# Kernel optimization log

Measured on AMD Instinct MI355X. Metric: run time of the kernel, lower is better.

The kernel has to match this reference:

```python
import jax, jax.numpy as jnp
import numpy as np

SEQ, BATCH, IN_DIM, HID, LAYERS, OUT = 512, 64, 512, 1024, 4, 1


def setup_inputs() -> dict:
    key = jax.random.key(0)
    ks = jax.random.split(key, 8)
    s = 1.0 / np.sqrt(HID)  # PyTorch default init range
    u = lambda k, shape: jax.random.uniform(k, shape, jnp.float32, -s, s)
    return {
        "x": jax.random.normal(ks[0], (SEQ, BATCH, IN_DIM), jnp.float32),
        "w_ih0": u(ks[1], (4 * HID, IN_DIM)),
        "w_ih_rest": u(ks[2], (LAYERS - 1, 4 * HID, HID)),
        "w_hh": u(ks[3], (LAYERS, 4 * HID, HID)),
        "b_ih": u(ks[4], (LAYERS, 4 * HID)),
        "b_hh": u(ks[5], (LAYERS, 4 * HID)),
        "fc_w": u(ks[6], (OUT, HID)),
        "fc_b": u(ks[7], (OUT,)),
    }


def _lstm_layer(xs, w_ih, w_hh, b):
    # xs: [T, B, D]; PyTorch gate order: i, f, g, o
    T, B, _ = xs.shape
    H = w_hh.shape[1]
    gx = jnp.einsum("tbd,gd->tbg", xs, w_ih) + b  # precompute input GEMM [T,B,4H]

    def step(carry, g_t):
        h, c = carry
        g = g_t + h @ w_hh.T
        i, f, gg, o = jnp.split(g, 4, axis=-1)
        c = jax.nn.sigmoid(f) * c + jax.nn.sigmoid(i) * jnp.tanh(gg)
        h = jax.nn.sigmoid(o) * jnp.tanh(c)
        return (h, c), h

    init = (jnp.zeros((B, H), xs.dtype), jnp.zeros((B, H), xs.dtype))
    _, hs = jax.lax.scan(step, init, gx)
    return hs  # [T, B, H]


def reference(x, w_ih0, w_ih_rest, w_hh, b_ih, b_hh, fc_w, fc_b):
    h = _lstm_layer(x, w_ih0, w_hh[0], b_ih[0] + b_hh[0])
    for l in range(1, LAYERS):
        h = _lstm_layer(h, w_ih_rest[l - 1], w_hh[l], b_ih[l] + b_hh[l])
    # Faithful to original: output is seq-first [T,B,H], and x[:, -1, :]
    # selects the LAST BATCH element over all timesteps -> [T, H]
    last = jax.nn.sigmoid(h[:, -1, :])
    return last @ fc_w.T + fc_b  # [T, OUT]
```

## Files before the change

### kernel.cpp

```cpp
#include <hip/hip_runtime.h>


typedef unsigned short u16;
typedef short bf16x8 __attribute__((ext_vector_type(8)));
typedef float f32x4 __attribute__((ext_vector_type(4)));
typedef float f32x16 __attribute__((ext_vector_type(16)));

__device__ __forceinline__ u16 f2bf(float f) {
  unsigned u = __float_as_uint(f);
  return (u16)((u + 0x7FFFu + ((u >> 16) & 1u)) >> 16);
}
__device__ __forceinline__ float bf2f(u16 s) {
  return __uint_as_float(((unsigned)s) << 16);
}
__device__ __forceinline__ bf16x8 ld8(const u16* p) {
  uint4 v = *(const uint4*)p;
  return __builtin_bit_cast(bf16x8, v);
}
__device__ __forceinline__ float sigf(float x) {
  x = fminf(fmaxf(x, -30.f), 30.f);
  return 1.f / (1.f + __expf(-x));
}
__device__ __forceinline__ float tanhf_(float x) {
  x = fminf(fmaxf(x, -15.f), 15.f);
  float e = __expf(-2.f * x);
  return (1.f - e) / (1.f + e);
}

#define AT_LD(p) __hip_atomic_load((p), __ATOMIC_RELAXED, __HIP_MEMORY_SCOPE_AGENT)
#define AT_ST(p, v) __hip_atomic_store((p), (v), __ATOMIC_RELAXED, __HIP_MEMORY_SCOPE_AGENT)

__global__ void repack_w(const float* __restrict__ wih0, const float* __restrict__ wihr,
                         const float* __restrict__ whh, u16* __restrict__ WCAT) {
  size_t i = (size_t)blockIdx.x * 256 + threadIdx.x;
  int l = (int)(i >> 23);
  int r = (int)(i >> 11) & 4095;
  int c = (int)i & 2047;
  int Kx = l ? 1024 : 512;
  float v = 0.f;
  if (c < Kx) v = l ? wihr[((size_t)(l - 1) * 4096 + r) * 1024 + c]
                    : wih0[(size_t)r * 512 + c];
  else if (c < Kx + 1024) v = whh[((size_t)l * 4096 + r) * 1024 + (c - Kx)];
  WCAT[i] = f2bf(v);
}

__global__ void repack_x(const float* __restrict__ x, u16* __restrict__ XP) {
  int i = blockIdx.x * 256 + threadIdx.x;
  int t = i >> 12, r = i & 4095, kc = r >> 6, b = r & 63;
  const float* src = x + ((size_t)t * 64 + b) * 512 + kc * 8;
  float4 v0 = *(const float4*)src, v1 = *(const float4*)(src + 4);
  u16 o[8] = {f2bf(v0.x), f2bf(v0.y), f2bf(v0.z), f2bf(v0.w),
              f2bf(v1.x), f2bf(v1.y), f2bf(v1.z), f2bf(v1.w)};
  *(uint4*)(XP + ((size_t)(t * 64 + kc) * 64 + b) * 8) = *(uint4*)o;
}

__global__ void bias_add(const float* __restrict__ a, const float* __restrict__ b,
                         float* __restrict__ o) {
  int i = blockIdx.x * blockDim.x + threadIdx.x;
  o[i] = a[i] + b[i];
}

template <int NF, int FX>
__device__ __forceinline__ void run_pipe(
    int layer, int w64, const u16* __restrict__ WCAT, const u16* __restrict__ XP,
    u16* __restrict__ HR, u16* __restrict__ HOUT, const float* __restrict__ BIAS,
    unsigned* __restrict__ FLAG, unsigned* __restrict__ EPOCH, float* R) {
  const int tid = threadIdx.x;
  const int lane = tid & 63, wv = tid >> 6;
  const int ks = wv & 3, nh = wv >> 2;
  const int l31 = lane & 31, lhi = lane >> 5;
  const int W = layer * 64 + w64;

  bf16x8 wf[NF];
  {
    const int lr = nh * 32 + l31;
    const int grow = (lr >> 4) * 1024 + 16 * w64 + (lr & 15);
    const u16* wrow = WCAT + ((size_t)layer * 4096 + grow) * 2048;
#pragma unroll
    for (int kk = 0; kk < NF; ++kk) {
      int f = ks * NF + kk;
      wf[kk] = ld8(wrow + f * 16 + lhi * 8);
    }
  }

  const int u = tid & 15, bp = tid >> 4;
  const int col = 16 * w64 + u;
  float c0 = 0.f, c1 = 0.f;
  const float bi = BIAS[layer * 4096 + col];
  const float bf_ = BIAS[layer * 4096 + 1024 + col];
  const float bg = BIAS[layer * 4096 + 2048 + col];
  const float bo = BIAS[layer * 4096 + 3072 + col];

  const int lane_base = (lhi * 64 + l31) * 8;
  u16* HRL = HR + (size_t)layer * 2097152;
  const u16* M0B = (NF == 32) ? HR + (size_t)(layer - 1) * 2097152 : XP;
  const int lrD = nh * 32 + l31;

  for (int s = 0; s < 515; ++s) {
    const int t = s - layer;
    const bool active = (t >= 0) && (t < 512);
    if (active) {
      *(f32x4*)&R[tid * 8] = f32x4{0.f, 0.f, 0.f, 0.f};
      *(f32x4*)&R[tid * 8 + 4] = f32x4{0.f, 0.f, 0.f, 0.f};
      __syncthreads();

      const u16* P0 = M0B + ((NF == 32) ? (size_t)(t & 31) * 65536
                                        : (size_t)t * 32768) + lane_base;
      const u16* P1 = HRL + (size_t)((t - 1) & 31) * 65536 + lane_base - (size_t)FX * 1024;

      f32x16 acc0 = {}, acc1 = {};
      uint4 a0[4], a1[4];
#pragma unroll
      for (int p = 0; p < 4; ++p) {
        int f = ks * NF + p;
        const u16* ap = (f < FX ? P0 : P1) + (size_t)f * 1024;
        a0[p] = *(const uint4*)ap;
        a1[p] = *(const uint4*)(ap + 256);
      }
#pragma unroll
      for (int kk = 0; kk < NF; ++kk) {
        uint4 ca = a0[kk & 3], cb = a1[kk & 3];
        if (kk + 4 < NF) {
          int f = ks * NF + kk + 4;
          const u16* ap = (f < FX ? P0 : P1) + (size_t)f * 1024;
          a0[kk & 3] = *(const uint4*)ap;
          a1[kk & 3] = *(const uint4*)(ap + 256);
        }
        acc0 = __builtin_amdgcn_mfma_f32_32x32x16_bf16(
            __builtin_bit_cast(bf16x8, ca), wf[kk], acc0, 0, 0, 0);
        acc1 = __builtin_amdgcn_mfma_f32_32x32x16_bf16(
            __builtin_bit_cast(bf16x8, cb), wf[kk], acc1, 0, 0, 0);
      }
#pragma unroll
      for (int r = 0; r < 16; ++r) {
        int m = (r & 3) + 8 * (r >> 2) + 4 * lhi;
        atomicAdd(&R[m * 64 + lrD], acc0[r]);
        atomicAdd(&R[(32 + m) * 64 + lrD], acc1[r]);
      }
      __syncthreads();
      {
        float p0i = R[bp * 64 + u] + bi, p0f = R[bp * 64 + 16 + u] + bf_;
        float p0g = R[bp * 64 + 32 + u] + bg, p0o = R[bp * 64 + 48 + u] + bo;
        float p1i = R[(bp + 32) * 64 + u] + bi, p1f = R[(bp + 32) * 64 + 16 + u] + bf_;
        float p1g = R[(bp + 32) * 64 + 32 + u] + bg, p1o = R[(bp + 32) * 64 + 48 + u] + bo;
        c0 = sigf(p0f) * c0 + sigf(p0i) * tanhf_(p0g);
        float h0 = sigf(p0o) * tanhf_(c0);
        c1 = sigf(p1f) * c1 + sigf(p1i) * tanhf_(p1g);
        float h1 = sigf(p1o) * tanhf_(c1);
        u16 hb0 = f2bf(h0), hb1 = f2bf(h1);
        unsigned n0 = (unsigned)(u16)__shfl_down((int)(unsigned)hb0, 1, 64);
        unsigned n1 = (unsigned)(u16)__shfl_down((int)(unsigned)hb1, 1, 64);
        if ((u & 1) == 0) {
          unsigned pk0 = (unsigned)hb0 | (n0 << 16);
          unsigned pk1 = (unsigned)hb1 | (n1 << 16);
          u16* slot = HRL + (size_t)(t & 31) * 65536;
          size_t e0 = ((size_t)(col >> 3) * 64 + bp) * 8 + (col & 7);
          AT_ST((unsigned*)(slot + e0), pk0);
          AT_ST((unsigned*)(slot + e0 + 256), pk1);
          if (layer == 3 && bp == 31)
            *(unsigned*)(HOUT + (size_t)t * 1024 + col) = pk1;
        }
      }
      __syncthreads();
    }
    const unsigned tgt = (unsigned)(s + 1);
    if (tid == 0) AT_ST(&FLAG[W * 64], tgt);
    if (W == 0) {
      if (wv == 0) {
        for (;;) {
          unsigned f0 = AT_LD(&FLAG[lane * 64]);
          unsigned f1 = AT_LD(&FLAG[(lane + 64) * 64]);
          unsigned f2 = AT_LD(&FLAG[(lane + 128) * 64]);
          unsigned f3 = AT_LD(&FLAG[(lane + 192) * 64]);
          bool ok = (f0 >= tgt) & (f1 >= tgt) & (f2 >= tgt) & (f3 >= tgt);
          if (__ballot(ok) == ~0ull) break;
          __builtin_amdgcn_s_sleep(1);
        }
        if (lane < 32) AT_ST(&EPOCH[lane * 64], tgt);
      }
    } else if (wv == 0) {
      unsigned* ep = &EPOCH[(W & 31) * 64];
      while (AT_LD(ep) < tgt) __builtin_amdgcn_s_sleep(1);
    }
    __syncthreads();
  }
}

__global__ __launch_bounds__(512, 2) void lstm_pipe(
    const u16* __restrict__ WCAT, const u16* __restrict__ XP,
    u16* __restrict__ HR, u16* __restrict__ HOUT,
    const float* __restrict__ BIAS, unsigned* __restrict__ FLAG,
    unsigned* __restrict__ EPOCH) {
  __shared__ float R[64 * 64];
  const int w = blockIdx.x;
  const int layer = w >> 6, w64 = w & 63;
  if (layer == 0) run_pipe<24, 32>(0, w64, WCAT, XP, HR, HOUT, BIAS, FLAG, EPOCH, R);
  else            run_pipe<32, 64>(layer, w64, WCAT, XP, HR, HOUT, BIAS, FLAG, EPOCH, R);
}

__global__ void lstm_head(const u16* __restrict__ Hl, const float* __restrict__ fcw,
                          const float* __restrict__ fcb, float* __restrict__ out) {
  int t = blockIdx.x, tid = threadIdx.x;
  const u16* hrow = Hl + (size_t)t * 1024;
  float s = 0.f;
  for (int j = tid; j < 1024; j += 256)
    s += sigf(bf2f(hrow[j])) * fcw[j];
  for (int o = 32; o; o >>= 1) s += __shfl_down(s, o, 64);
  __shared__ float red[4];
  if ((tid & 63) == 0) red[tid >> 6] = s;
  __syncthreads();
  if (tid == 0) out[t] = red[0] + red[1] + red[2] + red[3] + fcb[0];
}

extern "C" void kernel_launch(void* const* d_in, const int* in_sizes, int n_in,
                              void* d_out, int out_size, void* d_ws, size_t ws_size,
                              hipStream_t stream) {
  const float* x    = (const float*)d_in[0];
  const float* wih0 = (const float*)d_in[1];
  const float* wihr = (const float*)d_in[2];
  const float* whh  = (const float*)d_in[3];
  const float* bih  = (const float*)d_in[4];
  const float* bhh  = (const float*)d_in[5];
  const float* fcw  = (const float*)d_in[6];
  const float* fcb  = (const float*)d_in[7];
  float* out = (float*)d_out;

  char* ws = (char*)d_ws;
  size_t off = 0;
  auto alc = [&](size_t b) { void* p = ws + off; off = (off + b + 255) & ~(size_t)255; return p; };
  u16* WCAT  = (u16*)alc(33554432ull * 2);
  u16* XP    = (u16*)alc(16777216ull * 2);
  u16* HR    = (u16*)alc(8388608ull * 2);
  u16* HOUT  = (u16*)alc(524288ull * 2);
  float* BIAS = (float*)alc(16384 * 4);
  unsigned* FLAG  = (unsigned*)alc(256 * 64 * 4);
  unsigned* EPOCH = (unsigned*)alc(32 * 64 * 4);
  (void)ws_size; (void)in_sizes; (void)n_in; (void)out_size;

  hipMemsetAsync(HR, 0, 8388608ull * 2, stream);
  hipMemsetAsync(FLAG, 0, 256 * 64 * 4, stream);
  hipMemsetAsync(EPOCH, 0, 32 * 64 * 4, stream);
  repack_w<<<dim3(131072), 256, 0, stream>>>(wih0, wihr, whh, WCAT);
  repack_x<<<dim3(8192), 256, 0, stream>>>(x, XP);
  bias_add<<<dim3(64), 256, 0, stream>>>(bih, bhh, BIAS);

  void* args[] = {&WCAT, &XP, &HR, &HOUT, &BIAS, &FLAG, &EPOCH};
  hipLaunchCooperativeKernel((const void*)lstm_pipe, dim3(256), dim3(512),
                             args, 0, stream);

  lstm_head<<<dim3(512), 256, 0, stream>>>(HOUT, fcw, fcb, out);
}
```

Measured before the change: 14.78 ms.

## Replace global grid barrier with per-layer dataflow flags in LSTM wavefront pipeline

Removes the centralized per-step grid barrier, where block 0 polled all flags and broadcast an epoch. Each block now waits only on its own layer's flags from the previous step, the next layer's ring-buffer consumption (a 31-step slack window), and the previous layer's flag for the current step. It also splits the GEMM so the recurrent h@W_hh part runs before waiting on the lower layer's output, overlapping that wait with compute. Block-to-layer mapping is interleaved, and weight fragments are reordered into recurrent and input parts. The risks are spin-wait contention from busy polling without sleep, and correctness depending on the ring-buffer slack logic.

```diff
diff --git a/kernel.cpp b/kernel.cpp
--- a/kernel.cpp
+++ b/kernel.cpp
@@ -60,27 +60,26 @@
   o[i] = a[i] + b[i];
 }
 
-template <int NF, int FX>
+template <int NFX>
 __device__ __forceinline__ void run_pipe(
     int layer, int w64, const u16* __restrict__ WCAT, const u16* __restrict__ XP,
     u16* __restrict__ HR, u16* __restrict__ HOUT, const float* __restrict__ BIAS,
-    unsigned* __restrict__ FLAG, unsigned* __restrict__ EPOCH, float* R) {
+    unsigned* __restrict__ FLAG, float* R) {
   const int tid = threadIdx.x;
   const int lane = tid & 63, wv = tid >> 6;
   const int ks = wv & 3, nh = wv >> 2;
   const int l31 = lane & 31, lhi = lane >> 5;
-  const int W = layer * 64 + w64;
-
-  bf16x8 wf[NF];
+  const int FX = NFX * 4;
+
+  bf16x8 wfc[NFX], wfo[16];
   {
     const int lr = nh * 32 + l31;
     const int grow = (lr >> 4) * 1024 + 16 * w64 + (lr & 15);
     const u16* wrow = WCAT + ((size_t)layer * 4096 + grow) * 2048;
 #pragma unroll
-    for (int kk = 0; kk < NF; ++kk) {
-      int f = ks * NF + kk;
-      wf[kk] = ld8(wrow + f * 16 + lhi * 8);
-    }
+    for (int j = 0; j < NFX; ++j) wfc[j] = ld8(wrow + (j * 4 + ks) * 16 + lhi * 8);
+#pragma unroll
+    for (int j = 0; j < 16; ++j) wfo[j] = ld8(wrow + (FX + j * 4 + ks) * 16 + lhi * 8);
   }
 
   const int u = tid & 15, bp = tid >> 4;
@@ -93,109 +92,121 @@
 
   const int lane_base = (lhi * 64 + l31) * 8;
   u16* HRL = HR + (size_t)layer * 2097152;
-  const u16* M0B = (NF == 32) ? HR + (size_t)(layer - 1) * 2097152 : XP;
+  const u16* HRm1 = (layer > 0) ? HR + (size_t)(layer - 1) * 2097152 : XP;
   const int lrD = nh * 32 + l31;
 
-  for (int s = 0; s < 515; ++s) {
-    const int t = s - layer;
-    const bool active = (t >= 0) && (t < 512);
-    if (active) {
-      *(f32x4*)&R[tid * 8] = f32x4{0.f, 0.f, 0.f, 0.f};
-      *(f32x4*)&R[tid * 8 + 4] = f32x4{0.f, 0.f, 0.f, 0.f};
-      __syncthreads();
-
-      const u16* P0 = M0B + ((NF == 32) ? (size_t)(t & 31) * 65536
-                                        : (size_t)t * 32768) + lane_base;
-      const u16* P1 = HRL + (size_t)((t - 1) & 31) * 65536 + lane_base - (size_t)FX * 1024;
-
-      f32x16 acc0 = {}, acc1 = {};
+  for (int t = 0; t < 512; ++t) {
+    *(f32x4*)&R[tid * 8] = f32x4{0.f, 0.f, 0.f, 0.f};
+    *(f32x4*)&R[tid * 8 + 4] = f32x4{0.f, 0.f, 0.f, 0.f};
+    if (wv == 0) {
+      for (;;) {
+        int f1 = (int)AT_LD(&FLAG[layer * 64 + lane]);
+        bool ok = (f1 >= t);
+        if (layer < 3) {
+          int f2 = (int)AT_LD(&FLAG[(layer + 1) * 64 + lane]);
+          ok &= (f2 >= t - 31);
+        }
+        if (__ballot(ok) == ~0ull) break;
+      }
+    }
+    __syncthreads();
+
+    f32x16 acc0 = {}, acc1 = {};
+    {
+      const u16* PO = HRL + (size_t)((t - 1) & 31) * 65536 + lane_base;
       uint4 a0[4], a1[4];
 #pragma unroll
       for (int p = 0; p < 4; ++p) {
-        int f = ks * NF + p;
-        const u16* ap = (f < FX ? P0 : P1) + (size_t)f * 1024;
-        a0[p] = *(const uint4*)ap;
-        a1[p] = *(const uint4*)(ap + 256);
-      }
-#pragma unroll
-      for (int kk = 0; kk < NF; ++kk) {
-        uint4 ca = a0[kk & 3], cb = a1[kk & 3];
-        if (kk + 4 < NF) {
-          int f = ks * NF + kk + 4;
-          const u16* ap = (f < FX ? P0 : P1) + (size_t)f * 1024;
-          a0[kk & 3] = *(const uint4*)ap;
-          a1[kk & 3] = *(const uint4*)(ap + 256);
+        const u16* ap = PO + (size_t)(p * 4 + ks) * 1024;
+        a0[p] = *(const uint4*)ap; a1[p] = *(const uint4*)(ap + 256);
+      }
+#pragma unroll
+      for (int j = 0; j < 16; ++j) {
+        uint4 ca = a0[j & 3], cb = a1[j & 3];
+        if (j + 4 < 16) {
+          const u16* ap = PO + (size_t)((j + 4) * 4 + ks) * 1024;
+          a0[j & 3] = *(const uint4*)ap; a1[j & 3] = *(const uint4*)(ap + 256);
         }
         acc0 = __builtin_amdgcn_mfma_f32_32x32x16_bf16(
-            __builtin_bit_cast(bf16x8, ca), wf[kk], acc0, 0, 0, 0);
+            __builtin_bit_cast(bf16x8, ca), wfo[j], acc0, 0, 0, 0);
         acc1 = __builtin_amdgcn_mfma_f32_32x32x16_bf16(
-            __builtin_bit_cast(bf16x8, cb), wf[kk], acc1, 0, 0, 0);
-      }
-#pragma unroll
-      for (int r = 0; r < 16; ++r) {
-        int m = (r & 3) + 8 * (r >> 2) + 4 * lhi;
-        atomicAdd(&R[m * 64 + lrD], acc0[r]);
-        atomicAdd(&R[(32 + m) * 64 + lrD], acc1[r]);
-      }
-      __syncthreads();
-      {
-        float p0i = R[bp * 64 + u] + bi, p0f = R[bp * 64 + 16 + u] + bf_;
-        float p0g = R[bp * 64 + 32 + u] + bg, p0o = R[bp * 64 + 48 + u] + bo;
-        float p1i = R[(bp + 32) * 64 + u] + bi, p1f = R[(bp + 32) * 64 + 16 + u] + bf_;
-        float p1g = R[(bp + 32) * 64 + 32 + u] + bg, p1o = R[(bp + 32) * 64 + 48 + u] + bo;
-        c0 = sigf(p0f) * c0 + sigf(p0i) * tanhf_(p0g);
-        float h0 = sigf(p0o) * tanhf_(c0);
-        c1 = sigf(p1f) * c1 + sigf(p1i) * tanhf_(p1g);
-        float h1 = sigf(p1o) * tanhf_(c1);
-        u16 hb0 = f2bf(h0), hb1 = f2bf(h1);
-        unsigned n0 = (unsigned)(u16)__shfl_down((int)(unsigned)hb0, 1, 64);
-        unsigned n1 = (unsigned)(u16)__shfl_down((int)(unsigned)hb1, 1, 64);
-        if ((u & 1) == 0) {
-          unsigned pk0 = (unsigned)hb0 | (n0 << 16);
-          unsigned pk1 = (unsigned)hb1 | (n1 << 16);
-          u16* slot = HRL + (size_t)(t & 31) * 65536;
-          size_t e0 = ((size_t)(col >> 3) * 64 + bp) * 8 + (col & 7);
-          AT_ST((unsigned*)(slot + e0), pk0);
-          AT_ST((unsigned*)(slot + e0 + 256), pk1);
-          if (layer == 3 && bp == 31)
-            *(unsigned*)(HOUT + (size_t)t * 1024 + col) = pk1;
+            __builtin_bit_cast(bf16x8, cb), wfo[j], acc1, 0, 0, 0);
+      }
+    }
+    if (layer > 0 && wv == 0) {
+      for (;;) {
+        int f = (int)AT_LD(&FLAG[(layer - 1) * 64 + lane]);
+        if (__ballot(f >= t + 1) == ~0ull) break;
+      }
+    }
+    __syncthreads();
+    {
+      const u16* PC = HRm1 + ((layer > 0) ? (size_t)(t & 31) * 65536
+                                          : (size_t)t * 32768) + lane_base;
+      uint4 a0[4], a1[4];
+#pragma unroll
+      for (int p = 0; p < 4; ++p) {
+        const u16* ap = PC + (size_t)(p * 4 + ks) * 1024;
+        a0[p] = *(const uint4*)ap; a1[p] = *(const uint4*)(ap + 256);
+      }
+#pragma unroll
+      for (int j = 0; j < NFX; ++j) {
+        uint4 ca = a0[j & 3], cb = a1[j & 3];
+        if (j + 4 < NFX) {
+          const u16* ap = PC + (size_t)((j + 4) * 4 + ks) * 1024;
+          a0[j & 3] = *(const uint4*)ap; a1[j & 3] = *(const uint4*)(ap + 256);
         }
-      }
-      __syncthreads();
-    }
-    const unsigned tgt = (unsigned)(s + 1);
-    if (tid == 0) AT_ST(&FLAG[W * 64], tgt);
-    if (W == 0) {
-      if (wv == 0) {
-        for (;;) {
-          unsigned f0 = AT_LD(&FLAG[lane * 64]);
-          unsigned f1 = AT_LD(&FLAG[(lane + 64) * 64]);
-          unsigned f2 = AT_LD(&FLAG[(lane + 128) * 64]);
-          unsigned f3 = AT_LD(&FLAG[(lane + 192) * 64]);
-          bool ok = (f0 >= tgt) & (f1 >= tgt) & (f2 >= tgt) & (f3 >= tgt);
-          if (__ballot(ok) == ~0ull) break;
-          __builtin_amdgcn_s_sleep(1);
-        }
-        if (lane < 32) AT_ST(&EPOCH[lane * 64], tgt);
-      }
-    } else if (wv == 0) {
-      unsigned* ep = &EPOCH[(W & 31) * 64];
-      while (AT_LD(ep) < tgt) __builtin_amdgcn_s_sleep(1);
-    }
-    __syncthreads();
+        acc0 = __builtin_amdgcn_mfma_f32_32x32x16_bf16(
+            __builtin_bit_cast(bf16x8, ca), wfc[j], acc0, 0, 0, 0);
+        acc1 = __builtin_amdgcn_mfma_f32_32x32x16_bf16(
+            __builtin_bit_cast(bf16x8, cb), wfc[j], acc1, 0, 0, 0);
+      }
+    }
+#pragma unroll
+    for (int r = 0; r < 16; ++r) {
+      int m = (r & 3) + 8 * (r >> 2) + 4 * lhi;
+      atomicAdd(&R[m * 64 + lrD], acc0[r]);
+      atomicAdd(&R[(32 + m) * 64 + lrD], acc1[r]);
+    }
+    __syncthreads();
+    {
+      float p0i = R[bp * 64 + u] + bi, p0f = R[bp * 64 + 16 + u] + bf_;
+      float p0g = R[bp * 64 + 32 + u] + bg, p0o = R[bp * 64 + 48 + u] + bo;
+      float p1i = R[(bp + 32) * 64 + u] + bi, p1f = R[(bp + 32) * 64 + 16 + u] + bf_;
+      float p1g = R[(bp + 32) * 64 + 32 + u] + bg, p1o = R[(bp + 32) * 64 + 48 + u] + bo;
+      c0 = sigf(p0f) * c0 + sigf(p0i) * tanhf_(p0g);
+      float h0 = sigf(p0o) * tanhf_(c0);
+      c1 = sigf(p1f) * c1 + sigf(p1i) * tanhf_(p1g);
+      float h1 = sigf(p1o) * tanhf_(c1);
+      u16 hb0 = f2bf(h0), hb1 = f2bf(h1);
+      unsigned n0 = (unsigned)(u16)__shfl_down((int)(unsigned)hb0, 1, 64);
+      unsigned n1 = (unsigned)(u16)__shfl_down((int)(unsigned)hb1, 1, 64);
+      if ((u & 1) == 0) {
+        unsigned pk0 = (unsigned)hb0 | (n0 << 16);
+        unsigned pk1 = (unsigned)hb1 | (n1 << 16);
+        u16* slot = HRL + (size_t)(t & 31) * 65536;
+        size_t e0 = ((size_t)(col >> 3) * 64 + bp) * 8 + (col & 7);
+        AT_ST((unsigned*)(slot + e0), pk0);
+        AT_ST((unsigned*)(slot + e0 + 256), pk1);
+        if (layer == 3 && bp == 31)
+          *(unsigned*)(HOUT + (size_t)t * 1024 + col) = pk1;
+      }
+    }
+    __syncthreads();
+    if (tid == 0) AT_ST(&FLAG[layer * 64 + w64], (unsigned)(t + 1));
   }
 }
 
 __global__ __launch_bounds__(512, 2) void lstm_pipe(
     const u16* __restrict__ WCAT, const u16* __restrict__ XP,
     u16* __restrict__ HR, u16* __restrict__ HOUT,
-    const float* __restrict__ BIAS, unsigned* __restrict__ FLAG,
-    unsigned* __restrict__ EPOCH) {
+    const float* __restrict__ BIAS, unsigned* __restrict__ FLAG) {
   __shared__ float R[64 * 64];
-  const int w = blockIdx.x;
-  const int layer = w >> 6, w64 = w & 63;
-  if (layer == 0) run_pipe<24, 32>(0, w64, WCAT, XP, HR, HOUT, BIAS, FLAG, EPOCH, R);
-  else            run_pipe<32, 64>(layer, w64, WCAT, XP, HR, HOUT, BIAS, FLAG, EPOCH, R);
+  const int b = blockIdx.x;
+  const int layer = (b & 7) >> 1;
+  const int w64 = (b >> 3) * 2 + (b & 1);
+  if (layer == 0) run_pipe<8>(0, w64, WCAT, XP, HR, HOUT, BIAS, FLAG, R);
+  else            run_pipe<16>(layer, w64, WCAT, XP, HR, HOUT, BIAS, FLAG, R);
 }
 
 __global__ void lstm_head(const u16* __restrict__ Hl, const float* __restrict__ fcw,
@@ -233,18 +244,16 @@
   u16* HR    = (u16*)alc(8388608ull * 2);
   u16* HOUT  = (u16*)alc(524288ull * 2);
   float* BIAS = (float*)alc(16384 * 4);
-  unsigned* FLAG  = (unsigned*)alc(256 * 64 * 4);
-  unsigned* EPOCH = (unsigned*)alc(32 * 64 * 4);
+  unsigned* FLAG = (unsigned*)alc(256 * 4);
   (void)ws_size; (void)in_sizes; (void)n_in; (void)out_size;
 
   hipMemsetAsync(HR, 0, 8388608ull * 2, stream);
-  hipMemsetAsync(FLAG, 0, 256 * 64 * 4, stream);
-  hipMemsetAsync(EPOCH, 0, 32 * 64 * 4, stream);
+  hipMemsetAsync(FLAG, 0, 256 * 4, stream);
   repack_w<<<dim3(131072), 256, 0, stream>>>(wih0, wihr, whh, WCAT);
   repack_x<<<dim3(8192), 256, 0, stream>>>(x, XP);
   bias_add<<<dim3(64), 256, 0, stream>>>(bih, bhh, BIAS);
 
-  void* args[] = {&WCAT, &XP, &HR, &HOUT, &BIAS, &FLAG, &EPOCH};
+  void* args[] = {&WCAT, &XP, &HR, &HOUT, &BIAS, &FLAG};
   hipLaunchCooperativeKernel((const void*)lstm_pipe, dim3(256), dim3(512),
                              args, 0, stream);
 
```

Measured after the change: 16.34 ms. 10.5% more time.
